# Kernel tuning notes

Hardware: AMD Instinct MI355X
Metric: run time of the kernel (lower is better)

Reference implementation:

```python
import jax, jax.numpy as jnp
import numpy as np

PRIOR_SCALE = 0.1
LOG_PS = float(np.log(PRIOR_SCALE))
NEG_SLOPE = 0.01  # nn.LeakyReLU default


def _kl_mean(mu, log_sigma, axes):
    # kl_div(mu_q, lsq, 0, lsp) = lsp - lsq + (exp(lsq)^2 + mu^2)/(2*exp(lsp)^2) - 0.5, mean over param dims
    kl = LOG_PS - log_sigma + (jnp.exp(log_sigma) ** 2 + mu ** 2) / (2.0 * PRIOR_SCALE ** 2) - 0.5
    return jnp.mean(kl, axis=axes)  # -> per-feature [F]


def _bayes_linear(x, wmu, wls, bmu, bls, ew, eb):
    # x: [B,F,Din], wmu/wls/ew: [F,Din,Dout], bmu/bls/eb: [F,Dout]
    W = wmu + jnp.exp(wls) * ew
    b = bmu + jnp.exp(bls) * eb
    out = jnp.einsum('bfi,fio->bfo', x, W) + b[None, :, :]
    kl_f = _kl_mean(wmu, wls, (1, 2)) + _kl_mean(bmu, bls, (1,))  # [F]
    return out, kl_f


def setup_inputs() -> dict:
    key = jax.random.key(0)
    ks = jax.random.split(key, 20)
    B, F, H = 16384, 64, 64
    inp = {
        'f': jax.random.normal(ks[0], (B, F), jnp.float32),
        'wmu0': jax.random.normal(ks[1], (F, 1, H), jnp.float32),
        'wls0': jax.random.normal(ks[2], (F, 1, H), jnp.float32),
        'bmu0': jax.random.normal(ks[3], (F, H), jnp.float32),
        'bls0': jax.random.normal(ks[4], (F, H), jnp.float32),
        'ew0': jax.random.normal(ks[5], (F, 1, H), jnp.float32),
        'eb0': jax.random.normal(ks[6], (F, H), jnp.float32),
        'wmu1': jax.random.normal(ks[7], (F, H, H), jnp.float32),
        'wls1': jax.random.normal(ks[8], (F, H, H), jnp.float32),
        'bmu1': jax.random.normal(ks[9], (F, H), jnp.float32),
        'bls1': jax.random.normal(ks[10], (F, H), jnp.float32),
        'ew1': jax.random.normal(ks[11], (F, H, H), jnp.float32),
        'eb1': jax.random.normal(ks[12], (F, H), jnp.float32),
        'wmu2': jax.random.normal(ks[13], (F, H, 1), jnp.float32),
        'wls2': jax.random.normal(ks[14], (F, H, 1), jnp.float32),
        'bmu2': jax.random.normal(ks[15], (F, 1), jnp.float32),
        'bls2': jax.random.normal(ks[16], (F, 1), jnp.float32),
        'ew2': jax.random.normal(ks[17], (F, H, 1), jnp.float32),
        'eb2': jax.random.normal(ks[18], (F, 1), jnp.float32),
        'bias': jnp.zeros((1,), jnp.float32),
    }
    return inp


def reference(f, wmu0, wls0, bmu0, bls0, ew0, eb0,
              wmu1, wls1, bmu1, bls1, ew1, eb1,
              wmu2, wls2, bmu2, bls2, ew2, eb2, bias):
    x = f[:, :, None]  # [B,F,1] (per-feature scalar input)
    out, kl0 = _bayes_linear(x, wmu0, wls0, bmu0, bls0, ew0, eb0)
    out = jax.nn.leaky_relu(out, NEG_SLOPE)
    out, kl1 = _bayes_linear(out, wmu1, wls1, bmu1, bls1, ew1, eb1)
    out = jax.nn.leaky_relu(out, NEG_SLOPE)  # dropout p=0 -> identity
    out, kl2 = _bayes_linear(out, wmu2, wls2, bmu2, bls2, ew2, eb2)  # [B,F,1]
    kl_total = jnp.sum(kl0 + kl1 + kl2)  # sum over features of per-feature kl sums
    conc = out[:, :, 0]  # concat of per-feature scalar outputs -> [B,F]
    y = jnp.sum(conc, axis=-1) + bias[0]  # feature_dropout p=0 -> identity
    return y, kl_total
```

## Files before the change

kernel.cpp:

```cpp
#include <hip/hip_runtime.h>
#include <hip/hip_fp16.h>

typedef _Float16 f16x8 __attribute__((ext_vector_type(8)));
typedef float floatx4 __attribute__((ext_vector_type(4)));

#define NEG 0.01f
#define KL_C (-2.8025850929940457f)

#define W0HOFF 131072
#define B0HOFF 133120
#define B1OFF  135168
#define W2OFF  139264
#define B2OFF  143360
#define KLPOFF 143424

__global__ void bayesnam_prep(const float* __restrict__ wmu0, const float* __restrict__ wls0,
                              const float* __restrict__ bmu0, const float* __restrict__ bls0,
                              const float* __restrict__ ew0,  const float* __restrict__ eb0,
                              const float* __restrict__ wmu1, const float* __restrict__ wls1,
                              const float* __restrict__ bmu1, const float* __restrict__ bls1,
                              const float* __restrict__ ew1,  const float* __restrict__ eb1,
                              const float* __restrict__ wmu2, const float* __restrict__ wls2,
                              const float* __restrict__ bmu2, const float* __restrict__ bls2,
                              const float* __restrict__ ew2,  const float* __restrict__ eb2,
                              const float* __restrict__ bias,
                              float* __restrict__ ws, float* __restrict__ out) {
    const int tid = threadIdx.x;
    const int bx  = blockIdx.x;
    __shared__ float red[256];
    if (bx < 128) {
        const int f  = bx >> 1;
        const int kk = bx & 1;
        __shared__ float w1s[32 * 65];
        const size_t base = (size_t)f * 4096 + (size_t)kk * 2048;
        float klacc = 0.f;
        #pragma unroll
        for (int i = 0; i < 8; ++i) {
            const int idx = i * 256 + tid;
            const float m = wmu1[base + idx];
            const float l = wls1[base + idx];
            const float e = ew1[base + idx];
            const float ex = expf(l);
            w1s[(idx >> 6) * 65 + (idx & 63)] = fmaf(ex, e, m);
            klacc += (KL_C - l) + 50.f * fmaf(ex, ex, m * m);
        }
        red[tid] = klacc * 0.000244140625f;
        __syncthreads();
        for (int s = 128; s > 0; s >>= 1) {
            if (tid < s) red[tid] += red[tid + s];
            __syncthreads();
        }
        if (tid == 0) ws[KLPOFF + bx] = red[0];
        const int lane = tid & 63;
        const int n    = tid >> 6;
        const int k0   = (lane >> 4) << 3;
        const int col  = n * 16 + (lane & 15);
        union { _Float16 h[8]; uint4 u; } fr;
        #pragma unroll
        for (int j = 0; j < 8; ++j) fr.h[j] = (_Float16)w1s[(k0 + j) * 65 + col];
        ((uint4*)ws)[(size_t)f * 512 + kk * 256 + tid] = fr.u;
    } else {
        float klacc = 0.f;
        _Float16* w0h = (_Float16*)(ws + W0HOFF);
        _Float16* b0h = (_Float16*)(ws + B0HOFF);
        for (int idx = (bx - 128) * 256 + tid; idx < 16448; idx += 2048) {
            const float *mu, *ls, *ew;
            int j, kind; float scale;
            if (idx < 4096)       { j = idx;         mu = wmu0; ls = wls0; ew = ew0; scale = 0.015625f; kind = 0; }
            else if (idx < 8192)  { j = idx - 4096;  mu = bmu0; ls = bls0; ew = eb0; scale = 0.015625f; kind = 1; }
            else if (idx < 12288) { j = idx - 8192;  mu = bmu1; ls = bls1; ew = eb1; scale = 0.015625f; kind = 2; }
            else if (idx < 16384) { j = idx - 12288; mu = wmu2; ls = wls2; ew = ew2; scale = 0.015625f; kind = 3; }
            else                  { j = idx - 16384; mu = bmu2; ls = bls2; ew = eb2; scale = 1.0f;      kind = 4; }
            const float m = mu[j], l = ls[j], e = ew[j];
            const float ex = expf(l);
            const float w  = fmaf(ex, e, m);
            if (kind == 0)      w0h[j] = (_Float16)w;
            else if (kind == 1) b0h[j] = (_Float16)w;
            else if (kind == 2) ws[B1OFF + j] = w;
            else if (kind == 3) ws[W2OFF + j] = w;
            else                ws[B2OFF + j] = w;
            klacc += scale * ((KL_C - l) + 50.f * fmaf(ex, ex, m * m));
        }
        const float bv = bias[0];
        for (int i = (bx - 128) * 256 + tid; i < 16384; i += 2048) out[i] = bv;
        red[tid] = klacc;
        __syncthreads();
        for (int s = 128; s > 0; s >>= 1) {
            if (tid < s) red[tid] += red[tid + s];
            __syncthreads();
        }
        if (tid == 0) ws[KLPOFF + 128 + (bx - 128)] = red[0];
    }
}

__global__ __launch_bounds__(256, 4) void bayesnam_main(const float* __restrict__ fin,
                                                        const float* __restrict__ ws,
                                                        float* __restrict__ out) {
    const int tid = threadIdx.x;
    const int l   = tid & 63;
    const int wid = tid >> 6;
    const int l15 = l & 15;
    const int lg  = l >> 4;
    const int rowbase = blockIdx.x * 128 + wid * 32;
    const int f0 = blockIdx.y * 4;

    if (blockIdx.x == 0 && blockIdx.y == 0 && tid < 64) {
        float k = 0.f;
        #pragma unroll
        for (int i = 0; i < 3; ++i) {
            const int p = tid + i * 64;
            if (p < 136) k += ws[KLPOFF + p];
        }
        k += __shfl_xor(k, 32, 64); k += __shfl_xor(k, 16, 64); k += __shfl_xor(k, 8, 64);
        k += __shfl_xor(k, 4, 64);  k += __shfl_xor(k, 2, 64);  k += __shfl_xor(k, 1, 64);
        if (tid == 0) out[16384] = k;
    }

    const uint4* __restrict__ w1q = (const uint4*)ws;
    const _Float16* __restrict__ w0h = (const _Float16*)(ws + W0HOFF);
    const _Float16* __restrict__ b0h = (const _Float16*)(ws + B0HOFF);
    const _Float16 negh = (_Float16)0.01f;

    const floatx4 x0v = *(const floatx4*)(fin + (size_t)(rowbase + l15) * 64 + f0);
    const floatx4 x1v = *(const floatx4*)(fin + (size_t)(rowbase + 16 + l15) * 64 + f0);

    float yacc[2][4];
    #pragma unroll
    for (int r = 0; r < 2; ++r)
        #pragma unroll
        for (int q = 0; q < 4; ++q) yacc[r][q] = 0.f;
    float b2sum = 0.f;

    #pragma unroll 1
    for (int fi = 0; fi < 4; ++fi) {
        const int f = f0 + fi;
        const float* b1p = ws + B1OFF + f * 64;
        const float* w2p = ws + W2OFF + f * 64;
        const _Float16 x0h = (_Float16)x0v[fi];
        const _Float16 x1h = (_Float16)x1v[fi];

        floatx4 acc[2][4];
        #pragma unroll
        for (int n = 0; n < 4; ++n) {
            const float bv = b1p[n * 16 + l15];
            acc[0][n] = floatx4{bv, bv, bv, bv};
            acc[1][n] = floatx4{bv, bv, bv, bv};
        }

        #pragma unroll
        for (int kk = 0; kk < 2; ++kk) {
            const int kb = kk * 32 + lg * 8;
            union HU { uint4 u; f16x8 v; };
            HU wu, bu;
            wu.u = *(const uint4*)(w0h + f * 64 + kb);
            bu.u = *(const uint4*)(b0h + f * 64 + kb);

            f16x8 t0 = wu.v * x0h + bu.v;
            f16x8 a0 = __builtin_elementwise_max(t0, t0 * negh);
            f16x8 t1 = wu.v * x1h + bu.v;
            f16x8 a1 = __builtin_elementwise_max(t1, t1 * negh);

            const uint4* bp = w1q + (size_t)(f * 8 + kk * 4) * 64 + l;
            #pragma unroll
            for (int n = 0; n < 4; ++n) {
                HU bf; bf.u = bp[n * 64];
                acc[0][n] = __builtin_amdgcn_mfma_f32_16x16x32_f16(a0, bf.v, acc[0][n], 0, 0, 0);
                acc[1][n] = __builtin_amdgcn_mfma_f32_16x16x32_f16(a1, bf.v, acc[1][n], 0, 0, 0);
            }
        }

        #pragma unroll
        for (int n = 0; n < 4; ++n) {
            const float w2v = w2p[n * 16 + l15];
            #pragma unroll
            for (int r = 0; r < 2; ++r)
                #pragma unroll
                for (int q = 0; q < 4; ++q) {
                    float v = acc[r][n][q];
                    v = fmaxf(v, NEG * v);
                    yacc[r][q] = fmaf(v, w2v, yacc[r][q]);
                }
        }
        b2sum += ws[B2OFF + f];
    }

    #pragma unroll
    for (int r = 0; r < 2; ++r)
        #pragma unroll
        for (int q = 0; q < 4; ++q) {
            float v = yacc[r][q];
            v += __shfl_xor(v, 1, 64);
            v += __shfl_xor(v, 2, 64);
            v += __shfl_xor(v, 4, 64);
            v += __shfl_xor(v, 8, 64);
            yacc[r][q] = v;
        }
    if (l15 == 0) {
        #pragma unroll
        for (int r = 0; r < 2; ++r)
            #pragma unroll
            for (int q = 0; q < 4; ++q)
                atomicAdd(&out[rowbase + r * 16 + lg * 4 + q], yacc[r][q] + b2sum);
    }
}

extern "C" void kernel_launch(void* const* d_in, const int* in_sizes, int n_in,
                              void* d_out, int out_size, void* d_ws, size_t ws_size,
                              hipStream_t stream) {
    const float* fin  = (const float*)d_in[0];
    const float* wmu0 = (const float*)d_in[1];
    const float* wls0 = (const float*)d_in[2];
    const float* bmu0 = (const float*)d_in[3];
    const float* bls0 = (const float*)d_in[4];
    const float* ew0  = (const float*)d_in[5];
    const float* eb0  = (const float*)d_in[6];
    const float* wmu1 = (const float*)d_in[7];
    const float* wls1 = (const float*)d_in[8];
    const float* bmu1 = (const float*)d_in[9];
    const float* bls1 = (const float*)d_in[10];
    const float* ew1  = (const float*)d_in[11];
    const float* eb1  = (const float*)d_in[12];
    const float* wmu2 = (const float*)d_in[13];
    const float* wls2 = (const float*)d_in[14];
    const float* bmu2 = (const float*)d_in[15];
    const float* bls2 = (const float*)d_in[16];
    const float* ew2  = (const float*)d_in[17];
    const float* eb2  = (const float*)d_in[18];
    const float* bias = (const float*)d_in[19];

    float* ws  = (float*)d_ws;
    float* out = (float*)d_out;

    hipLaunchKernelGGL(bayesnam_prep, dim3(136), dim3(256), 0, stream,
                       wmu0, wls0, bmu0, bls0, ew0, eb0,
                       wmu1, wls1, bmu1, bls1, ew1, eb1,
                       wmu2, wls2, bmu2, bls2, ew2, eb2,
                       bias, ws, out);

    hipLaunchKernelGGL(bayesnam_main, dim3(128, 16), dim3(256), 0, stream,
                       fin, ws, out);
}
```

Baseline: 32.00 us.

## Stage W1 MFMA fragments in LDS via direct loads and widen prep grid

The main kernel now copies the four features' fp16 W1 fragments (32 KB) into shared memory with global_load_lds before compute, and the MFMA loop reads B operands from LDS instead of global memory. The prep kernel splits the W1 transform over 256 blocks instead of 128 for more parallelism, with the KL partial count and layout indices adjusted to match. This aims to cut repeated global/L2 fragment loads and to shorten the prep stage. In exchange it uses large LDS per block, which may limit occupancy, and adds a block-wide barrier.

```diff
diff --git a/kernel.cpp b/kernel.cpp
--- a/kernel.cpp
+++ b/kernel.cpp
@@ -28,14 +28,14 @@
     const int tid = threadIdx.x;
     const int bx  = blockIdx.x;
     __shared__ float red[256];
-    if (bx < 128) {
-        const int f  = bx >> 1;
-        const int kk = bx & 1;
-        __shared__ float w1s[32 * 65];
-        const size_t base = (size_t)f * 4096 + (size_t)kk * 2048;
+    if (bx < 256) {
+        const int f = bx >> 2;
+        const int q = bx & 3;
+        __shared__ float w1s[16 * 65];
+        const size_t base = (size_t)f * 4096 + (size_t)q * 1024;
         float klacc = 0.f;
         #pragma unroll
-        for (int i = 0; i < 8; ++i) {
+        for (int i = 0; i < 4; ++i) {
             const int idx = i * 256 + tid;
             const float m = wmu1[base + idx];
             const float l = wls1[base + idx];
@@ -51,19 +51,25 @@
             __syncthreads();
         }
         if (tid == 0) ws[KLPOFF + bx] = red[0];
-        const int lane = tid & 63;
-        const int n    = tid >> 6;
-        const int k0   = (lane >> 4) << 3;
-        const int col  = n * 16 + (lane & 15);
-        union { _Float16 h[8]; uint4 u; } fr;
-        #pragma unroll
-        for (int j = 0; j < 8; ++j) fr.h[j] = (_Float16)w1s[(k0 + j) * 65 + col];
-        ((uint4*)ws)[(size_t)f * 512 + kk * 256 + tid] = fr.u;
+        if (tid < 128) {
+            const int n   = tid >> 5;
+            const int ls  = tid & 31;
+            const int s   = ls >> 4;
+            const int l15 = ls & 15;
+            const int lg  = 2 * (q & 1) + s;
+            const int lane = lg * 16 + l15;
+            const int kk  = q >> 1;
+            const int col = n * 16 + l15;
+            union { _Float16 h[8]; uint4 u; } fr;
+            #pragma unroll
+            for (int j = 0; j < 8; ++j) fr.h[j] = (_Float16)w1s[(8 * s + j) * 65 + col];
+            ((uint4*)ws)[(size_t)f * 512 + kk * 256 + n * 64 + lane] = fr.u;
+        }
     } else {
         float klacc = 0.f;
         _Float16* w0h = (_Float16*)(ws + W0HOFF);
         _Float16* b0h = (_Float16*)(ws + B0HOFF);
-        for (int idx = (bx - 128) * 256 + tid; idx < 16448; idx += 2048) {
+        for (int idx = (bx - 256) * 256 + tid; idx < 16448; idx += 2048) {
             const float *mu, *ls, *ew;
             int j, kind; float scale;
             if (idx < 4096)       { j = idx;         mu = wmu0; ls = wls0; ew = ew0; scale = 0.015625f; kind = 0; }
@@ -82,20 +88,21 @@
             klacc += scale * ((KL_C - l) + 50.f * fmaf(ex, ex, m * m));
         }
         const float bv = bias[0];
-        for (int i = (bx - 128) * 256 + tid; i < 16384; i += 2048) out[i] = bv;
+        for (int i = (bx - 256) * 256 + tid; i < 16384; i += 2048) out[i] = bv;
         red[tid] = klacc;
         __syncthreads();
         for (int s = 128; s > 0; s >>= 1) {
             if (tid < s) red[tid] += red[tid + s];
             __syncthreads();
         }
-        if (tid == 0) ws[KLPOFF + 128 + (bx - 128)] = red[0];
+        if (tid == 0) ws[KLPOFF + 256 + (bx - 256)] = red[0];
     }
 }
 
 __global__ __launch_bounds__(256, 4) void bayesnam_main(const float* __restrict__ fin,
                                                         const float* __restrict__ ws,
                                                         float* __restrict__ out) {
+    __shared__ uint4 fragLDS[2048];
     const int tid = threadIdx.x;
     const int l   = tid & 63;
     const int wid = tid >> 6;
@@ -104,25 +111,38 @@
     const int rowbase = blockIdx.x * 128 + wid * 32;
     const int f0 = blockIdx.y * 4;
 
+    {
+        const char* gsrc = (const char*)ws + (size_t)f0 * 8192;
+        #pragma unroll
+        for (int i = 0; i < 8; ++i) {
+            const int chunk = (wid * 8 + i) * 1024;
+            __builtin_amdgcn_global_load_lds(
+                (const __attribute__((address_space(1))) unsigned int*)(gsrc + chunk + l * 16),
+                (__attribute__((address_space(3))) unsigned int*)((char*)fragLDS + chunk),
+                16, 0, 0);
+        }
+    }
+
     if (blockIdx.x == 0 && blockIdx.y == 0 && tid < 64) {
         float k = 0.f;
         #pragma unroll
-        for (int i = 0; i < 3; ++i) {
+        for (int i = 0; i < 5; ++i) {
             const int p = tid + i * 64;
-            if (p < 136) k += ws[KLPOFF + p];
+            if (p < 264) k += ws[KLPOFF + p];
         }
         k += __shfl_xor(k, 32, 64); k += __shfl_xor(k, 16, 64); k += __shfl_xor(k, 8, 64);
         k += __shfl_xor(k, 4, 64);  k += __shfl_xor(k, 2, 64);  k += __shfl_xor(k, 1, 64);
         if (tid == 0) out[16384] = k;
     }
 
-    const uint4* __restrict__ w1q = (const uint4*)ws;
     const _Float16* __restrict__ w0h = (const _Float16*)(ws + W0HOFF);
     const _Float16* __restrict__ b0h = (const _Float16*)(ws + B0HOFF);
     const _Float16 negh = (_Float16)0.01f;
 
     const floatx4 x0v = *(const floatx4*)(fin + (size_t)(rowbase + l15) * 64 + f0);
     const floatx4 x1v = *(const floatx4*)(fin + (size_t)(rowbase + 16 + l15) * 64 + f0);
+
+    __syncthreads();
 
     float yacc[2][4];
     #pragma unroll
@@ -160,7 +180,7 @@
             f16x8 t1 = wu.v * x1h + bu.v;
             f16x8 a1 = __builtin_elementwise_max(t1, t1 * negh);
 
-            const uint4* bp = w1q + (size_t)(f * 8 + kk * 4) * 64 + l;
+            const uint4* bp = fragLDS + ((fi * 8 + kk * 4) * 64 + l);
             #pragma unroll
             for (int n = 0; n < 4; ++n) {
                 HU bf; bf.u = bp[n * 64];
@@ -231,7 +251,7 @@
     float* ws  = (float*)d_ws;
     float* out = (float*)d_out;
 
-    hipLaunchKernelGGL(bayesnam_prep, dim3(136), dim3(256), 0, stream,
+    hipLaunchKernelGGL(bayesnam_prep, dim3(264), dim3(256), 0, stream,
                        wmu0, wls0, bmu0, bls0, ew0, eb0,
                        wmu1, wls1, bmu1, bls1, ew1, eb1,
                        wmu2, wls2, bmu2, bls2, ew2, eb2,
```

Measured after the change: 30.83 us. -3.7%, faster.
